# Optimization experiments

Hardware: AMD Instinct MI355X
Metric: run time of the kernel (lower is better)

## Reference

```python
import jax, jax.numpy as jnp
import numpy as np

IRE = 1.0 / 400.0

def _stencil(f):
    # f: [B, C, X, Y]; returns (u,v) 5-point stencil fields, each [B, X-2, Y-2]
    m = f[:, :, 1:-1, 1:-1]
    l = f[:, :, :-2, 1:-1]
    r = f[:, :, 2:, 1:-1]
    b = f[:, :, 1:-1, :-2]
    t = f[:, :, 1:-1, 2:]
    return (m[:, 0], m[:, 1], l[:, 0], l[:, 1], r[:, 0], r[:, 1],
            b[:, 0], b[:, 1], t[:, 0], t[:, 1])

def _residuals(um, vm, ul, vl, ur, vr, ub, vb, ut, vt):
    dudx = (ur - ul) * 0.5
    dvdy = (vt - vb) * 0.5
    dudy = (ut - ub) * 0.5
    dvdx = (vr - vl) * 0.5
    du2dx = 0.25 * ((ur + um) ** 2 - (ul + um) ** 2)
    duvdy = 0.25 * ((ut + um) * (vt + vm) - (ub + um) * (vb + vm))
    dv2dy = 0.25 * ((vt + vm) ** 2 - (vb + vm) ** 2)
    dvudx = 0.25 * ((vr + vm) * (ur + um) - (vl + vm) * (ul + um))
    dudx2 = ur - um * 2 + ul
    dudy2 = ut - um * 2 + ub
    dvdx2 = vr - vm * 2 + vl
    dvdy2 = vt - vm * 2 + vb
    mass = dudx + dvdy
    mom_u = du2dx + duvdy - (dudx2 + dudy2) * IRE
    mom_v = dvudx + dv2dy - (dvdx2 + dvdy2) * IRE
    return mass, mom_u, mom_v, dudx, dudy, dvdx, dvdy

def setup_inputs() -> dict:
    key = jax.random.key(0)
    k1, k2 = jax.random.split(key)
    pred = jax.random.normal(k1, (64, 2, 512, 512), dtype=jnp.float32)
    trut = jax.random.normal(k2, (64, 2, 512, 512), dtype=jnp.float32)
    return {"pred": pred, "trut": trut}

def reference(pred, trut):
    mass_t, momu_t, momv_t, dudx_t, dudy_t, dvdx_t, dvdy_t = _residuals(*_stencil(trut))
    mass_p, momu_p, momv_p, dudx_p, dudy_p, dvdx_p, dvdy_p = _residuals(*_stencil(pred))
    lossMass = jnp.mean(jnp.abs(mass_t - mass_p))
    lossMom = jnp.mean(jnp.abs(momu_t - momu_p) + jnp.abs(momv_t - momv_p))
    lossGdl = jnp.mean(jnp.abs(dudx_t - dudx_p) + jnp.abs(dudy_t - dudy_p)
                       + jnp.abs(dvdx_t - dvdx_p) + jnp.abs(dvdy_t - dvdy_p)) / 4.0
    lossL1 = jnp.mean(jnp.abs(pred - trut))
    # lossGdl computed (as in original) but unused in the final combination
    del lossGdl
    return (lossMass * 5 + lossMom * 25 + lossL1) / 3
```

## Files before the change

### kernel.cpp

```cpp
#include <hip/hip_runtime.h>

#define IRE (1.0f / 400.0f)

constexpr int W = 512;
constexpr int H = 512;
constexpr int NB = 64;
constexpr int ROWS = 8;
constexpr int CHUNKS = H / ROWS;
constexpr int STRIPS = 2;
constexpr int GRID = NB * CHUNKS * STRIPS;

__device__ __forceinline__ void residuals3(
    float um, float vm, float ul, float vl, float ur, float vr,
    float ub, float vb, float ut, float vt,
    float& mass, float& momu, float& momv)
{
    float dudx = (ur - ul) * 0.5f;
    float dvdy = (vt - vb) * 0.5f;
    float ru = ur + um, lu = ul + um, tu_ = ut + um, bu = ub + um;
    float rv = vr + vm, lv = vl + vm, tv_ = vt + vm, bv = vb + vm;
    float du2dx = 0.25f * (ru * ru - lu * lu);
    float duvdy = 0.25f * (tu_ * tv_ - bu * bv);
    float dv2dy = 0.25f * (tv_ * tv_ - bv * bv);
    float dvudx = 0.25f * (rv * ru - lv * lu);
    float dudx2 = ur - 2.0f * um + ul;
    float dudy2 = ut - 2.0f * um + ub;
    float dvdx2 = vr - 2.0f * vm + vl;
    float dvdy2 = vt - 2.0f * vm + vb;
    mass = dudx + dvdy;
    momu = du2dx + duvdy - (dudx2 + dudy2) * IRE;
    momv = dvudx + dv2dy - (dvdx2 + dvdy2) * IRE;
}

__global__ __launch_bounds__(64) void loss_main(
    const float* __restrict__ pred, const float* __restrict__ trut,
    double* __restrict__ partial)
{
    const int lane = threadIdx.x;
    int bid = blockIdx.x;
    const int strip = bid % STRIPS; bid /= STRIPS;
    const int chunk = bid % CHUNKS; bid /= CHUNKS;
    const int b = bid;

    const int r0 = chunk * ROWS;
    const int js = strip * (64 * 4) + lane * 4;

    const size_t CH = (size_t)H * W;
    const float* g_tu = trut + (size_t)b * 2 * CH;
    const float* g_tv = g_tu + CH;
    const float* g_pu = pred + (size_t)b * 2 * CH;
    const float* g_pv = g_pu + CH;

    const int lo = (r0 > 0) ? r0 : 1;
    const int hi = (r0 + ROWS < H - 1) ? (r0 + ROWS) : (H - 1);

    float accMass = 0.0f, accMom = 0.0f, accL1 = 0.0f;

    float4 Ptu, Ptv, Ppu, Ppv;
    float4 Xtu, Xtv, Xpu, Xpv;
    float4 Ntu, Ntv, Npu, Npv;

    auto loadRow = [&](int r, float4& a, float4& bb, float4& c, float4& d) {
        const size_t off = (size_t)r * W + js;
        a  = *(const float4*)(g_tu + off);
        bb = *(const float4*)(g_tv + off);
        c  = *(const float4*)(g_pu + off);
        d  = *(const float4*)(g_pv + off);
        if (r >= r0 && r < r0 + ROWS) {
            accL1 += fabsf(c.x - a.x) + fabsf(c.y - a.y) + fabsf(c.z - a.z) + fabsf(c.w - a.w)
                   + fabsf(d.x - bb.x) + fabsf(d.y - bb.y) + fabsf(d.z - bb.z) + fabsf(d.w - bb.w);
        }
    };

    loadRow(lo - 1, Ptu, Ptv, Ppu, Ppv);
    loadRow(lo,     Xtu, Xtv, Xpu, Xpv);
    loadRow(lo + 1, Ntu, Ntv, Npu, Npv);

    for (int i = lo; i < hi; ++i) {
        float4 Qtu = {0,0,0,0}, Qtv = {0,0,0,0}, Qpu = {0,0,0,0}, Qpv = {0,0,0,0};
        if (i + 2 <= hi) loadRow(i + 2, Qtu, Qtv, Qpu, Qpv);

        float l_tu = __shfl_up(Xtu.w, 1);
        float l_tv = __shfl_up(Xtv.w, 1);
        float l_pu = __shfl_up(Xpu.w, 1);
        float l_pv = __shfl_up(Xpv.w, 1);
        float r_tu = __shfl_down(Xtu.x, 1);
        float r_tv = __shfl_down(Xtv.x, 1);
        float r_pu = __shfl_down(Xpu.x, 1);
        float r_pv = __shfl_down(Xpv.x, 1);
        if (lane == 0 && js > 0) {
            const size_t o = (size_t)i * W + js - 1;
            l_tu = g_tu[o]; l_tv = g_tv[o]; l_pu = g_pu[o]; l_pv = g_pv[o];
        }
        if (lane == 63 && js + 4 < W) {
            const size_t o = (size_t)i * W + js + 4;
            r_tu = g_tu[o]; r_tv = g_tv[o]; r_pu = g_pu[o]; r_pv = g_pv[o];
        }

        const float Ctu[6] = {l_tu, Xtu.x, Xtu.y, Xtu.z, Xtu.w, r_tu};
        const float Ctv[6] = {l_tv, Xtv.x, Xtv.y, Xtv.z, Xtv.w, r_tv};
        const float Cpu[6] = {l_pu, Xpu.x, Xpu.y, Xpu.z, Xpu.w, r_pu};
        const float Cpv[6] = {l_pv, Xpv.x, Xpv.y, Xpv.z, Xpv.w, r_pv};
        const float Pu[4] = {Ptu.x, Ptu.y, Ptu.z, Ptu.w};
        const float Pv[4] = {Ptv.x, Ptv.y, Ptv.z, Ptv.w};
        const float PU[4] = {Ppu.x, Ppu.y, Ppu.z, Ppu.w};
        const float PV[4] = {Ppv.x, Ppv.y, Ppv.z, Ppv.w};
        const float Nu[4] = {Ntu.x, Ntu.y, Ntu.z, Ntu.w};
        const float Nv[4] = {Ntv.x, Ntv.y, Ntv.z, Ntv.w};
        const float NU[4] = {Npu.x, Npu.y, Npu.z, Npu.w};
        const float NV[4] = {Npv.x, Npv.y, Npv.z, Npv.w};

        #pragma unroll
        for (int k = 0; k < 4; ++k) {
            const int j = js + k;
            if (j >= 1 && j <= W - 2) {
                float mT, uT, vT, mP, uP, vP;
                residuals3(Ctu[k+1], Ctv[k+1], Pu[k], Pv[k], Nu[k], Nv[k],
                           Ctu[k],   Ctv[k],   Ctu[k+2], Ctv[k+2], mT, uT, vT);
                residuals3(Cpu[k+1], Cpv[k+1], PU[k], PV[k], NU[k], NV[k],
                           Cpu[k],   Cpv[k],   Cpu[k+2], Cpv[k+2], mP, uP, vP);
                accMass += fabsf(mT - mP);
                accMom  += fabsf(uT - uP) + fabsf(vT - vP);
            }
        }

        Ptu = Xtu; Ptv = Xtv; Ppu = Xpu; Ppv = Xpv;
        Xtu = Ntu; Xtv = Ntv; Xpu = Npu; Xpv = Npv;
        Ntu = Qtu; Ntv = Qtv; Npu = Qpu; Npv = Qpv;
    }

    float res = 5.0f * accMass + 25.0f * accMom;
    float l1  = accL1;
    #pragma unroll
    for (int off = 32; off > 0; off >>= 1) {
        res += __shfl_down(res, off);
        l1  += __shfl_down(l1, off);
    }
    if (lane == 0) {
        partial[(size_t)blockIdx.x * 2 + 0] = (double)res;
        partial[(size_t)blockIdx.x * 2 + 1] = (double)l1;
    }
}

__global__ __launch_bounds__(256) void loss_final(
    const double* __restrict__ partial, float* __restrict__ out)
{
    __shared__ double sres[4], sl1[4];
    const int t = threadIdx.x;
    double res = 0.0, l1 = 0.0;
    for (int i = t; i < GRID; i += 256) {
        res += partial[(size_t)i * 2 + 0];
        l1  += partial[(size_t)i * 2 + 1];
    }
    #pragma unroll
    for (int off = 32; off > 0; off >>= 1) {
        res += __shfl_down(res, off);
        l1  += __shfl_down(l1, off);
    }
    const int wave = t >> 6;
    if ((t & 63) == 0) { sres[wave] = res; sl1[wave] = l1; }
    __syncthreads();
    if (t == 0) {
        res = sres[0] + sres[1] + sres[2] + sres[3];
        l1  = sl1[0] + sl1[1] + sl1[2] + sl1[3];
        const double nRes = 64.0 * 510.0 * 510.0;
        const double nL1  = 64.0 * 2.0 * 512.0 * 512.0;
        out[0] = (float)((res / nRes + l1 / nL1) / 3.0);
    }
}

extern "C" void kernel_launch(void* const* d_in, const int* in_sizes, int n_in,
                              void* d_out, int out_size, void* d_ws, size_t ws_size,
                              hipStream_t stream)
{
    const float* pred = (const float*)d_in[0];
    const float* trut = (const float*)d_in[1];
    double* partial = (double*)d_ws;
    loss_main<<<GRID, 64, 0, stream>>>(pred, trut, partial);
    loss_final<<<1, 256, 0, stream>>>(partial, (float*)d_out);
}
```

Before: 297.8 us.

## Give each wave a full 512-column row to drop strip halos

Each lane now handles 8 contiguous columns, loaded as two float4 per field, so a single 64-lane wave spans the whole row. The column strips go away, and with them the divergent scalar global loads that lane 0 and lane 63 used to fetch left and right halo values. The grid halves while per-thread work and register use double, and launch bounds now request 4 waves per SIMD. The conditional prefetch of the next row becomes an unconditional load that re-reads row hi on the last iteration and skips the L1 term there, which keeps control flow uniform at the cost of one redundant row load.

```diff
diff --git a/kernel.cpp b/kernel.cpp
--- a/kernel.cpp
+++ b/kernel.cpp
@@ -7,8 +7,11 @@
 constexpr int NB = 64;
 constexpr int ROWS = 8;
 constexpr int CHUNKS = H / ROWS;
-constexpr int STRIPS = 2;
-constexpr int GRID = NB * CHUNKS * STRIPS;
+constexpr int GRID = NB * CHUNKS;
+
+struct Row {
+    float4 tu0, tu1, tv0, tv1, pu0, pu1, pv0, pv1;
+};
 
 __device__ __forceinline__ void residuals3(
     float um, float vm, float ul, float vl, float ur, float vr,
@@ -32,18 +35,15 @@
     momv = dvudx + dv2dy - (dvdx2 + dvdy2) * IRE;
 }
 
-__global__ __launch_bounds__(64) void loss_main(
+__global__ __launch_bounds__(64, 4) void loss_main(
     const float* __restrict__ pred, const float* __restrict__ trut,
     double* __restrict__ partial)
 {
-    const int lane = threadIdx.x;
-    int bid = blockIdx.x;
-    const int strip = bid % STRIPS; bid /= STRIPS;
-    const int chunk = bid % CHUNKS; bid /= CHUNKS;
-    const int b = bid;
-
+    const int lane  = threadIdx.x;
+    const int chunk = blockIdx.x % CHUNKS;
+    const int b     = blockIdx.x / CHUNKS;
     const int r0 = chunk * ROWS;
-    const int js = strip * (64 * 4) + lane * 4;
+    const int c0 = lane * 8;
 
     const size_t CH = (size_t)H * W;
     const float* g_tu = trut + (size_t)b * 2 * CH;
@@ -56,77 +56,72 @@
 
     float accMass = 0.0f, accMom = 0.0f, accL1 = 0.0f;
 
-    float4 Ptu, Ptv, Ppu, Ppv;
-    float4 Xtu, Xtv, Xpu, Xpv;
-    float4 Ntu, Ntv, Npu, Npv;
+    Row P, X, N;
 
-    auto loadRow = [&](int r, float4& a, float4& bb, float4& c, float4& d) {
-        const size_t off = (size_t)r * W + js;
-        a  = *(const float4*)(g_tu + off);
-        bb = *(const float4*)(g_tv + off);
-        c  = *(const float4*)(g_pu + off);
-        d  = *(const float4*)(g_pv + off);
-        if (r >= r0 && r < r0 + ROWS) {
-            accL1 += fabsf(c.x - a.x) + fabsf(c.y - a.y) + fabsf(c.z - a.z) + fabsf(c.w - a.w)
-                   + fabsf(d.x - bb.x) + fabsf(d.y - bb.y) + fabsf(d.z - bb.z) + fabsf(d.w - bb.w);
+    auto loadRow = [&](int r, Row& R, bool countL1) {
+        const size_t off = (size_t)r * W + c0;
+        R.tu0 = *(const float4*)(g_tu + off);  R.tu1 = *(const float4*)(g_tu + off + 4);
+        R.tv0 = *(const float4*)(g_tv + off);  R.tv1 = *(const float4*)(g_tv + off + 4);
+        R.pu0 = *(const float4*)(g_pu + off);  R.pu1 = *(const float4*)(g_pu + off + 4);
+        R.pv0 = *(const float4*)(g_pv + off);  R.pv1 = *(const float4*)(g_pv + off + 4);
+        if (countL1 && r >= r0 && r < r0 + ROWS) {
+            accL1 += fabsf(R.pu0.x - R.tu0.x) + fabsf(R.pu0.y - R.tu0.y)
+                   + fabsf(R.pu0.z - R.tu0.z) + fabsf(R.pu0.w - R.tu0.w)
+                   + fabsf(R.pu1.x - R.tu1.x) + fabsf(R.pu1.y - R.tu1.y)
+                   + fabsf(R.pu1.z - R.tu1.z) + fabsf(R.pu1.w - R.tu1.w)
+                   + fabsf(R.pv0.x - R.tv0.x) + fabsf(R.pv0.y - R.tv0.y)
+                   + fabsf(R.pv0.z - R.tv0.z) + fabsf(R.pv0.w - R.tv0.w)
+                   + fabsf(R.pv1.x - R.tv1.x) + fabsf(R.pv1.y - R.tv1.y)
+                   + fabsf(R.pv1.z - R.tv1.z) + fabsf(R.pv1.w - R.tv1.w);
         }
     };
 
-    loadRow(lo - 1, Ptu, Ptv, Ppu, Ppv);
-    loadRow(lo,     Xtu, Xtv, Xpu, Xpv);
-    loadRow(lo + 1, Ntu, Ntv, Npu, Npv);
+    loadRow(lo - 1, P, true);
+    loadRow(lo,     X, true);
+    loadRow(lo + 1, N, true);
 
     for (int i = lo; i < hi; ++i) {
-        float4 Qtu = {0,0,0,0}, Qtv = {0,0,0,0}, Qpu = {0,0,0,0}, Qpv = {0,0,0,0};
-        if (i + 2 <= hi) loadRow(i + 2, Qtu, Qtv, Qpu, Qpv);
+        Row Q;
+        const bool pf = (i + 2 <= hi);
+        loadRow(pf ? (i + 2) : hi, Q, pf);
 
-        float l_tu = __shfl_up(Xtu.w, 1);
-        float l_tv = __shfl_up(Xtv.w, 1);
-        float l_pu = __shfl_up(Xpu.w, 1);
-        float l_pv = __shfl_up(Xpv.w, 1);
-        float r_tu = __shfl_down(Xtu.x, 1);
-        float r_tv = __shfl_down(Xtv.x, 1);
-        float r_pu = __shfl_down(Xpu.x, 1);
-        float r_pv = __shfl_down(Xpv.x, 1);
-        if (lane == 0 && js > 0) {
-            const size_t o = (size_t)i * W + js - 1;
-            l_tu = g_tu[o]; l_tv = g_tv[o]; l_pu = g_pu[o]; l_pv = g_pv[o];
-        }
-        if (lane == 63 && js + 4 < W) {
-            const size_t o = (size_t)i * W + js + 4;
-            r_tu = g_tu[o]; r_tv = g_tv[o]; r_pu = g_pu[o]; r_pv = g_pv[o];
-        }
+        float Ltu = __shfl_up(X.tu1.w, 1), Rtu = __shfl_down(X.tu0.x, 1);
+        float Ltv = __shfl_up(X.tv1.w, 1), Rtv = __shfl_down(X.tv0.x, 1);
+        float Lpu = __shfl_up(X.pu1.w, 1), Rpu = __shfl_down(X.pu0.x, 1);
+        float Lpv = __shfl_up(X.pv1.w, 1), Rpv = __shfl_down(X.pv0.x, 1);
 
-        const float Ctu[6] = {l_tu, Xtu.x, Xtu.y, Xtu.z, Xtu.w, r_tu};
-        const float Ctv[6] = {l_tv, Xtv.x, Xtv.y, Xtv.z, Xtv.w, r_tv};
-        const float Cpu[6] = {l_pu, Xpu.x, Xpu.y, Xpu.z, Xpu.w, r_pu};
-        const float Cpv[6] = {l_pv, Xpv.x, Xpv.y, Xpv.z, Xpv.w, r_pv};
-        const float Pu[4] = {Ptu.x, Ptu.y, Ptu.z, Ptu.w};
-        const float Pv[4] = {Ptv.x, Ptv.y, Ptv.z, Ptv.w};
-        const float PU[4] = {Ppu.x, Ppu.y, Ppu.z, Ppu.w};
-        const float PV[4] = {Ppv.x, Ppv.y, Ppv.z, Ppv.w};
-        const float Nu[4] = {Ntu.x, Ntu.y, Ntu.z, Ntu.w};
-        const float Nv[4] = {Ntv.x, Ntv.y, Ntv.z, Ntv.w};
-        const float NU[4] = {Npu.x, Npu.y, Npu.z, Npu.w};
-        const float NV[4] = {Npv.x, Npv.y, Npv.z, Npv.w};
+        const float ctu[10] = {Ltu, X.tu0.x, X.tu0.y, X.tu0.z, X.tu0.w,
+                                    X.tu1.x, X.tu1.y, X.tu1.z, X.tu1.w, Rtu};
+        const float ctv[10] = {Ltv, X.tv0.x, X.tv0.y, X.tv0.z, X.tv0.w,
+                                    X.tv1.x, X.tv1.y, X.tv1.z, X.tv1.w, Rtv};
+        const float cpu_[10]= {Lpu, X.pu0.x, X.pu0.y, X.pu0.z, X.pu0.w,
+                                    X.pu1.x, X.pu1.y, X.pu1.z, X.pu1.w, Rpu};
+        const float cpv[10] = {Lpv, X.pv0.x, X.pv0.y, X.pv0.z, X.pv0.w,
+                                    X.pv1.x, X.pv1.y, X.pv1.z, X.pv1.w, Rpv};
+        const float ptu[8] = {P.tu0.x, P.tu0.y, P.tu0.z, P.tu0.w, P.tu1.x, P.tu1.y, P.tu1.z, P.tu1.w};
+        const float ptv[8] = {P.tv0.x, P.tv0.y, P.tv0.z, P.tv0.w, P.tv1.x, P.tv1.y, P.tv1.z, P.tv1.w};
+        const float ppu[8] = {P.pu0.x, P.pu0.y, P.pu0.z, P.pu0.w, P.pu1.x, P.pu1.y, P.pu1.z, P.pu1.w};
+        const float ppv[8] = {P.pv0.x, P.pv0.y, P.pv0.z, P.pv0.w, P.pv1.x, P.pv1.y, P.pv1.z, P.pv1.w};
+        const float ntu[8] = {N.tu0.x, N.tu0.y, N.tu0.z, N.tu0.w, N.tu1.x, N.tu1.y, N.tu1.z, N.tu1.w};
+        const float ntv[8] = {N.tv0.x, N.tv0.y, N.tv0.z, N.tv0.w, N.tv1.x, N.tv1.y, N.tv1.z, N.tv1.w};
+        const float npu[8] = {N.pu0.x, N.pu0.y, N.pu0.z, N.pu0.w, N.pu1.x, N.pu1.y, N.pu1.z, N.pu1.w};
+        const float npv[8] = {N.pv0.x, N.pv0.y, N.pv0.z, N.pv0.w, N.pv1.x, N.pv1.y, N.pv1.z, N.pv1.w};
 
         #pragma unroll
-        for (int k = 0; k < 4; ++k) {
-            const int j = js + k;
+        for (int k = 0; k < 8; ++k) {
+            const int j = c0 + k;
             if (j >= 1 && j <= W - 2) {
                 float mT, uT, vT, mP, uP, vP;
-                residuals3(Ctu[k+1], Ctv[k+1], Pu[k], Pv[k], Nu[k], Nv[k],
-                           Ctu[k],   Ctv[k],   Ctu[k+2], Ctv[k+2], mT, uT, vT);
-                residuals3(Cpu[k+1], Cpv[k+1], PU[k], PV[k], NU[k], NV[k],
-                           Cpu[k],   Cpv[k],   Cpu[k+2], Cpv[k+2], mP, uP, vP);
+                residuals3(ctu[k+1], ctv[k+1], ptu[k], ptv[k], ntu[k], ntv[k],
+                           ctu[k],   ctv[k],   ctu[k+2], ctv[k+2], mT, uT, vT);
+                residuals3(cpu_[k+1], cpv[k+1], ppu[k], ppv[k], npu[k], npv[k],
+                           cpu_[k],   cpv[k],   cpu_[k+2], cpv[k+2], mP, uP, vP);
                 accMass += fabsf(mT - mP);
                 accMom  += fabsf(uT - uP) + fabsf(vT - vP);
             }
         }
 
-        Ptu = Xtu; Ptv = Xtv; Ppu = Xpu; Ppv = Xpv;
-        Xtu = Ntu; Xtv = Ntv; Xpu = Npu; Xpv = Npv;
-        Ntu = Qtu; Ntv = Qtv; Npu = Qpu; Npv = Qpv;
+        P = X; X = N; N = Q;
     }
 
     float res = 5.0f * accMass + 25.0f * accMom;
```

Measured after the change: 387.0 us. 1.3x slower.
